# Optimization experiments

Hardware: AMD Instinct MI355X
Metric: run time of the kernel (lower is better)

The kernel has to match this reference:

```python
import jax, jax.numpy as jnp
import numpy as np
import math

B, T, C = 2, 2048, 1024
H = 16            # n_head
RATIO = 4         # ratio_kv
HKV = H // RATIO  # n_head_kv = 4
HD = C // H       # head_dim = 64
G = H // HKV      # query heads per kv head = 4


def _alibi_slopes(n_heads):
    # n_heads must be a power of 2 here (H=16)
    assert math.log2(n_heads).is_integer()
    start = 2.0 ** (-(2.0 ** (-(math.log2(n_heads) - 3))))
    return np.array([start * (start ** i) for i in range(n_heads)], dtype=np.float32)


def setup_inputs() -> dict:
    key = jax.random.key(0)
    ks = jax.random.split(key, 5)
    return {
        "x": jax.random.normal(ks[0], (B, T, C), dtype=jnp.float32),
        "Wq": jax.random.normal(ks[1], (C, C), dtype=jnp.float32) * 0.02,
        "Wk": jax.random.normal(ks[2], (C, HKV * HD), dtype=jnp.float32) * 0.02,
        "Wv": jax.random.normal(ks[3], (C, HKV * HD), dtype=jnp.float32) * 0.02,
        "Wo": jax.random.normal(ks[4], (C, C), dtype=jnp.float32) * 0.02,
    }


def reference(x, Wq, Wk, Wv, Wo):
    # GQA causal attention with ALiBi bias (flash-disabled fallback path).
    # q: [B,HKV,G,T,HD] (grouped query heads), k/v: [B,HKV,T,HD]
    q = (x @ Wq).reshape(B, T, H, HD).transpose(0, 2, 1, 3).reshape(B, HKV, G, T, HD)
    k = (x @ Wk).reshape(B, T, HKV, HD).transpose(0, 2, 1, 3)
    v = (x @ Wv).reshape(B, T, HKV, HD).transpose(0, 2, 1, 3)

    scale = 1.0 / math.sqrt(HD)
    att = jnp.einsum('bkgtd,bksd->bkgts', q, k) * scale  # [B,HKV,G,T,T]

    # ALiBi: original repeats alibi(n_head) by G and truncates to n_head,
    # so query head h uses slope get_slopes(H)[h // G] == slopes[:HKV] per kv group.
    slopes = jnp.asarray(_alibi_slopes(H))[:HKV]          # [HKV]
    pos = jnp.arange(T)
    rel = (pos[None, :] - pos[:, None]).astype(jnp.float32)  # [T,T], rel[i,j]=j-i
    bias = slopes[:, None, None] * rel                    # [HKV,T,T]
    causal = jnp.triu(jnp.full((T, T), -jnp.inf, dtype=jnp.float32), 1)

    att = att + bias[None, :, None] + causal
    att = jax.nn.softmax(att.astype(jnp.float32), axis=-1).astype(q.dtype)

    y = jnp.einsum('bkgts,bksd->bkgtd', att, v)           # [B,HKV,G,T,HD]
    y = y.reshape(B, H, T, HD).transpose(0, 2, 1, 3).reshape(B, T, C)
    return y @ Wo
```

## Files before the change

kernel.cpp:

```cpp
#include <hip/hip_runtime.h>
#include <hip/hip_bf16.h>
#include <math.h>

#define B_ 2
#define T_ 2048
#define C_ 1024
#define H_ 16
#define HKV_ 4
#define G_ 4
#define HD_ 64
#define KVC_ 256
#define NQKV_ 1536
#define NQT_ 32

typedef __attribute__((ext_vector_type(8))) short bf16x8;
typedef __attribute__((ext_vector_type(4))) float f32x4;

static __device__ inline short f2bf(float f) {
    __hip_bfloat16 h = __float2bfloat16(f);
    short s;
    __builtin_memcpy(&s, &h, 2);
    return s;
}
static __device__ inline short f2bf_trunc(float f) {
    unsigned int u;
    __builtin_memcpy(&u, &f, 4);
    return (short)(u >> 16);
}
static __device__ inline float bf2f(short s) {
    unsigned int u = ((unsigned int)(unsigned short)s) << 16;
    float f;
    __builtin_memcpy(&f, &u, 4);
    return f;
}

static __device__ inline void gload_lds16(const short* g, short* lds) {
    __builtin_amdgcn_global_load_lds(
        (const __attribute__((address_space(1))) unsigned int*)g,
        (__attribute__((address_space(3))) unsigned int*)lds, 16, 0, 0);
}

__global__ __launch_bounds__(256) void cast_bf16(
    const float* __restrict__ in, short* __restrict__ out, int n)
{
    const int i = (blockIdx.x * 256 + threadIdx.x) * 8;
    if (i >= n) return;
    const float4 a = *(const float4*)(in + i);
    const float4 b = *(const float4*)(in + i + 4);
    bf16x8 o;
    o[0] = f2bf(a.x); o[1] = f2bf(a.y); o[2] = f2bf(a.z); o[3] = f2bf(a.w);
    o[4] = f2bf(b.x); o[5] = f2bf(b.y); o[6] = f2bf(b.z); o[7] = f2bf(b.w);
    *(bf16x8*)(out + i) = o;
}

__global__ __launch_bounds__(256) void w_transpose(
    const float* __restrict__ Wq, const float* __restrict__ Wk,
    const float* __restrict__ Wv, const float* __restrict__ Wo,
    short* __restrict__ Wt, short* __restrict__ Wot)
{
    const int z = blockIdx.z;
    const float* in;
    short* out;
    int N;
    if (z == 0)      { in = Wq; out = Wt;                     N = C_; }
    else if (z == 1) { in = Wk; out = Wt + C_ * C_;           N = KVC_; }
    else if (z == 2) { in = Wv; out = Wt + (C_ + KVC_) * C_;  N = KVC_; }
    else             { in = Wo; out = Wot;                    N = C_; }
    const int n0 = blockIdx.x * 32;
    if (n0 >= N) return;
    __shared__ float t[32][33];
    const int tx = threadIdx.x, ty = threadIdx.y;
    const int k0 = blockIdx.y * 32;
    #pragma unroll
    for (int j = 0; j < 4; j++)
        t[ty + j * 8][tx] = in[(size_t)(k0 + ty + j * 8) * N + n0 + tx];
    __syncthreads();
    #pragma unroll
    for (int j = 0; j < 4; j++)
        out[(size_t)(n0 + ty + j * 8) * C_ + k0 + tx] = f2bf(t[tx][ty + j * 8]);
}

template <bool OUT_BF16>
__global__ __launch_bounds__(256) void gemm_bf16(
    const short* __restrict__ A, const short* __restrict__ Bt,
    void* __restrict__ Cout, int M, int N, int K)
{
    __shared__ short As[2][128 * 32];
    __shared__ short Bs[2][128 * 32];
    const int tid = threadIdx.x;
    const int wave = tid >> 6, lane = tid & 63;
    const int l15 = lane & 15, quad = lane >> 4;
    const int row0 = blockIdx.y * 128, col0 = blockIdx.x * 128;
    const int wr = (wave >> 1) * 64, wc = (wave & 1) * 64;
    const int sr = lane >> 2, kof = (lane & 3) * 8;

    f32x4 acc[4][4];
    #pragma unroll
    for (int i = 0; i < 4; i++)
        #pragma unroll
        for (int j = 0; j < 4; j++)
            acc[i][j] = (f32x4){0.f, 0.f, 0.f, 0.f};

#define GSTAGE(KT, BUF) do {                                                   \
        _Pragma("unroll")                                                      \
        for (int i_ = 0; i_ < 2; i_++) {                                       \
            const int rr = i_ * 64 + wave * 16;                                \
            gload_lds16(A + (size_t)(row0 + rr + sr) * K + (KT) + kof,         \
                        &As[BUF][rr * 32]);                                    \
            gload_lds16(Bt + (size_t)(col0 + rr + sr) * K + (KT) + kof,        \
                        &Bs[BUF][rr * 32]);                                    \
        }                                                                      \
    } while (0)

    GSTAGE(0, 0);
    asm volatile("s_waitcnt vmcnt(0)" ::: "memory");
    __builtin_amdgcn_s_barrier();

    int cur = 0;
    const int nkt = K >> 5;
    for (int t = 0; t < nkt; ++t) {
        if (t + 1 < nkt) GSTAGE((t + 1) * 32, cur ^ 1);

        bf16x8 af[4], bfr[4];
        #pragma unroll
        for (int mt = 0; mt < 4; mt++)
            af[mt] = *(const bf16x8*)&As[cur][(wr + mt * 16 + l15) * 32 + quad * 8];
        #pragma unroll
        for (int nt = 0; nt < 4; nt++)
            bfr[nt] = *(const bf16x8*)&Bs[cur][(wc + nt * 16 + l15) * 32 + quad * 8];
        #pragma unroll
        for (int mt = 0; mt < 4; mt++)
            #pragma unroll
            for (int nt = 0; nt < 4; nt++)
                acc[mt][nt] = __builtin_amdgcn_mfma_f32_16x16x32_bf16(
                    af[mt], bfr[nt], acc[mt][nt], 0, 0, 0);

        asm volatile("s_waitcnt vmcnt(0)" ::: "memory");
        __builtin_amdgcn_s_barrier();
        cur ^= 1;
    }
#undef GSTAGE

    #pragma unroll
    for (int mt = 0; mt < 4; mt++) {
        #pragma unroll
        for (int r = 0; r < 4; r++) {
            const size_t row = row0 + wr + mt * 16 + quad * 4 + r;
            #pragma unroll
            for (int nt = 0; nt < 4; nt++) {
                const size_t col = col0 + wc + nt * 16 + l15;
                if (OUT_BF16)
                    ((short*)Cout)[row * N + col] = f2bf(acc[mt][nt][r]);
                else
                    ((float*)Cout)[row * N + col] = acc[mt][nt][r];
            }
        }
    }
}

__global__ __launch_bounds__(256) void kv_tile(
    const short* __restrict__ QKV, short* __restrict__ Kt, short* __restrict__ Vt)
{
    __shared__ short Ls[64 * 72];
    const int jt = blockIdx.x;
    const int bk = blockIdx.y;
    const int b = bk >> 2, kh = bk & 3;
    const int tid = threadIdx.x;
    const int key = tid >> 2, d16 = (tid & 3) * 16;
    const size_t src = (size_t)(b * T_ + jt * 64 + key) * NQKV_ + C_ + kh * 64 + d16;
    const size_t tbase = (size_t)(bk * 32 + jt) * 4096;

    {
        const int i = (key >> 4) * 2 + (d16 >> 5);
        const int qd = (d16 & 31) >> 3;
        short* dst = Kt + tbase + i * 512 + (qd * 16 + (key & 15)) * 8;
        *(bf16x8*)dst         = *(const bf16x8*)(QKV + src);
        *(bf16x8*)(dst + 128) = *(const bf16x8*)(QKV + src + 8);
    }
    *(bf16x8*)&Ls[key * 72 + d16]     = *(const bf16x8*)(QKV + src + KVC_);
    *(bf16x8*)&Ls[key * 72 + d16 + 8] = *(const bf16x8*)(QKV + src + KVC_ + 8);
    __syncthreads();
    const int d = tid >> 2, k16 = (tid & 3) * 16;
    bf16x8 o0, o1;
    #pragma unroll
    for (int i = 0; i < 8; i++) o0[i] = Ls[(k16 + i) * 72 + d];
    #pragma unroll
    for (int i = 0; i < 8; i++) o1[i] = Ls[(k16 + 8 + i) * 72 + d];
    {
        const int i = (d >> 4) * 2 + (k16 >> 5);
        const int qk = (k16 & 31) >> 3;
        short* dst = Vt + tbase + i * 512 + (qk * 16 + (d & 15)) * 8;
        *(bf16x8*)dst         = o0;
        *(bf16x8*)(dst + 128) = o1;
    }
}

#define LSTR 72

__global__ __launch_bounds__(256) void attn_mfma(
    const short* __restrict__ QKV, const short* __restrict__ Ktg,
    const short* __restrict__ Vtg, short* __restrict__ Y)
{
    const int qx = blockIdx.x;
    const int bh = blockIdx.y;
    const int qtL = qx, qtH = NQT_ - 1 - qx;
    const int b = bh >> 4, h = bh & 15, kh = h >> 2;
    const float slope2 = exp2f(-0.5f * (float)(kh + 1)) * 1.44269504f;
    const int tid = threadIdx.x;
    const int wave = tid >> 6, lane = tid & 63;
    const int l15 = lane & 15, quad = lane >> 4;

    __shared__ short Ps[4 * 32 * LSTR];
    short* Pw = &Ps[wave * 32 * LSTR];
    const int wswz = ((quad >> 1) & 1) << 4;
    const int rswz = ((l15 >> 3) & 1) << 4;

    const size_t bT = (size_t)b * T_;
    const size_t tb0 = (size_t)((b * HKV_ + kh) * 32) * 4096;
    const short* Kt = Ktg + tb0;
    const short* Vt = Vtg + tb0;
    const int qrow0H = qtH * 64 + wave * 16;
    const int qrow0L = qtL * 64 + wave * 16;

    const float qscale = 0.125f * 1.44269504f;
    bf16x8 qfH[2], qfL[2];
    #pragma unroll
    for (int k0 = 0; k0 < 2; k0++) {
        const short* qpH = QKV + (bT + qrow0H + l15) * NQKV_ + h * 64;
        const short* qpL = QKV + (bT + qrow0L + l15) * NQKV_ + h * 64;
        bf16x8 rH = *(const bf16x8*)(qpH + k0 * 32 + quad * 8);
        bf16x8 rL = *(const bf16x8*)(qpL + k0 * 32 + quad * 8);
        #pragma unroll
        for (int j = 0; j < 8; j++) {
            qfH[k0][j] = f2bf(bf2f(rH[j]) * qscale);
            qfL[k0][j] = f2bf(bf2f(rL[j]) * qscale);
        }
    }

    const short one_s = (short)0x3F80;
    const bf16x8 ones = {one_s, one_s, one_s, one_s, one_s, one_s, one_s, one_s};

    f32x4 OaccH[4], OaccL[4], laccH, laccL;
    #pragma unroll
    for (int nt = 0; nt < 4; nt++) {
        OaccH[nt] = (f32x4){0.f, 0.f, 0.f, 0.f};
        OaccL[nt] = (f32x4){0.f, 0.f, 0.f, 0.f};
    }
    laccH = (f32x4){0.f, 0.f, 0.f, 0.f};
    laccL = (f32x4){0.f, 0.f, 0.f, 0.f};

    bf16x8 kf[8], vf[8];
    #pragma unroll
    for (int i = 0; i < 8; i++)
        kf[i] = *(const bf16x8*)(Kt + i * 512 + lane * 8);
    #pragma unroll
    for (int i = 0; i < 8; i++)
        vf[i] = *(const bf16x8*)(Vt + i * 512 + lane * 8);

    for (int jtk = 0; jtk <= qtH; jtk++) {
        const bool doL = (jtk <= qtL);
        const int pjt = (jtk < qtH) ? jtk + 1 : qtH;

        f32x4 sH[4], sL[4];
        #pragma unroll
        for (int nt = 0; nt < 4; nt++) {
            f32x4 a = {0.f, 0.f, 0.f, 0.f};
            a = __builtin_amdgcn_mfma_f32_16x16x32_bf16(qfH[0], kf[nt*2+0], a, 0, 0, 0);
            a = __builtin_amdgcn_mfma_f32_16x16x32_bf16(qfH[1], kf[nt*2+1], a, 0, 0, 0);
            sH[nt] = a;
        }
        if (doL) {
            #pragma unroll
            for (int nt = 0; nt < 4; nt++) {
                f32x4 a = {0.f, 0.f, 0.f, 0.f};
                a = __builtin_amdgcn_mfma_f32_16x16x32_bf16(qfL[0], kf[nt*2+0], a, 0, 0, 0);
                a = __builtin_amdgcn_mfma_f32_16x16x32_bf16(qfL[1], kf[nt*2+1], a, 0, 0, 0);
                sL[nt] = a;
            }
        }

        #pragma unroll
        for (int i = 0; i < 8; i++)
            kf[i] = *(const bf16x8*)(Kt + (size_t)pjt * 4096 + i * 512 + lane * 8);

        {
            const float base = slope2 * (float)(jtk * 64 + l15 - quad * 4 - qrow0H);
            if (jtk == qtH) {
                #pragma unroll
                for (int nt = 0; nt < 4; nt++) {
                    const int colsw = ((nt * 16 + l15) ^ wswz);
                    #pragma unroll
                    for (int r = 0; r < 4; r++) {
                        const float relv = (float)(jtk * 64 + l15 - quad * 4 - qrow0H)
                                         + (float)(nt * 16 - r);
                        float p = __builtin_amdgcn_exp2f(
                            fmaf(slope2, (float)(nt * 16 - r), base) + sH[nt][r]);
                        if (relv > 0.f) p = 0.f;
                        Pw[(quad * 4 + r) * LSTR + colsw] = f2bf_trunc(p);
                    }
                }
            } else {
                #pragma unroll
                for (int nt = 0; nt < 4; nt++) {
                    const int colsw = ((nt * 16 + l15) ^ wswz);
                    #pragma unroll
                    for (int r = 0; r < 4; r++) {
                        float p = __builtin_amdgcn_exp2f(
                            fmaf(slope2, (float)(nt * 16 - r), base) + sH[nt][r]);
                        Pw[(quad * 4 + r) * LSTR + colsw] = f2bf_trunc(p);
                    }
                }
            }
        }
        if (doL) {
            const float base = slope2 * (float)(jtk * 64 + l15 - quad * 4 - qrow0L);
            if (jtk == qtL) {
                #pragma unroll
                for (int nt = 0; nt < 4; nt++) {
                    const int colsw = ((nt * 16 + l15) ^ wswz);
                    #pragma unroll
                    for (int r = 0; r < 4; r++) {
                        const float relv = (float)(jtk * 64 + l15 - quad * 4 - qrow0L)
                                         + (float)(nt * 16 - r);
                        float p = __builtin_amdgcn_exp2f(
                            fmaf(slope2, (float)(nt * 16 - r), base) + sL[nt][r]);
                        if (relv > 0.f) p = 0.f;
                        Pw[(16 + quad * 4 + r) * LSTR + colsw] = f2bf_trunc(p);
                    }
                }
            } else {
                #pragma unroll
                for (int nt = 0; nt < 4; nt++) {
                    const int colsw = ((nt * 16 + l15) ^ wswz);
                    #pragma unroll
                    for (int r = 0; r < 4; r++) {
                        float p = __builtin_amdgcn_exp2f(
                            fmaf(slope2, (float)(nt * 16 - r), base) + sL[nt][r]);
                        Pw[(16 + quad * 4 + r) * LSTR + colsw] = f2bf_trunc(p);
                    }
                }
            }
        }
        __asm__ volatile("s_waitcnt lgkmcnt(0)" ::: "memory");

        {
            bf16x8 pf0 = *(const bf16x8*)&Pw[l15 * LSTR + ((quad * 8) ^ rswz)];
            bf16x8 pf1 = *(const bf16x8*)&Pw[l15 * LSTR + ((32 + quad * 8) ^ rswz)];
            laccH = __builtin_amdgcn_mfma_f32_16x16x32_bf16(pf0, ones, laccH, 0, 0, 0);
            laccH = __builtin_amdgcn_mfma_f32_16x16x32_bf16(pf1, ones, laccH, 0, 0, 0);
            #pragma unroll
            for (int nt = 0; nt < 4; nt++) {
                OaccH[nt] = __builtin_amdgcn_mfma_f32_16x16x32_bf16(
                    pf0, vf[nt*2+0], OaccH[nt], 0, 0, 0);
                OaccH[nt] = __builtin_amdgcn_mfma_f32_16x16x32_bf16(
                    pf1, vf[nt*2+1], OaccH[nt], 0, 0, 0);
            }
        }
        if (doL) {
            bf16x8 pf0 = *(const bf16x8*)&Pw[(16 + l15) * LSTR + ((quad * 8) ^ rswz)];
            bf16x8 pf1 = *(const bf16x8*)&Pw[(16 + l15) * LSTR + ((32 + quad * 8) ^ rswz)];
            laccL = __builtin_amdgcn_mfma_f32_16x16x32_bf16(pf0, ones, laccL, 0, 0, 0);
            laccL = __builtin_amdgcn_mfma_f32_16x16x32_bf16(pf1, ones, laccL, 0, 0, 0);
            #pragma unroll
            for (int nt = 0; nt < 4; nt++) {
                OaccL[nt] = __builtin_amdgcn_mfma_f32_16x16x32_bf16(
                    pf0, vf[nt*2+0], OaccL[nt], 0, 0, 0);
                OaccL[nt] = __builtin_amdgcn_mfma_f32_16x16x32_bf16(
                    pf1, vf[nt*2+1], OaccL[nt], 0, 0, 0);
            }
        }

        #pragma unroll
        for (int i = 0; i < 8; i++)
            vf[i] = *(const bf16x8*)(Vt + (size_t)pjt * 4096 + i * 512 + lane * 8);
    }

    #pragma unroll
    for (int r = 0; r < 4; r++) {
        const float invH = 1.f / laccH[r];
        const float invL = 1.f / laccL[r];
        const int rowH = qrow0H + quad * 4 + r;
        const int rowL = qrow0L + quad * 4 + r;
        short* ypH = Y + (bT + rowH) * C_ + h * 64 + l15;
        short* ypL = Y + (bT + rowL) * C_ + h * 64 + l15;
        #pragma unroll
        for (int nt = 0; nt < 4; nt++) {
            ypH[nt * 16] = f2bf(OaccH[nt][r] * invH);
            ypL[nt * 16] = f2bf(OaccL[nt][r] * invL);
        }
    }
}

extern "C" void kernel_launch(void* const* d_in, const int* in_sizes, int n_in,
                              void* d_out, int out_size, void* d_ws, size_t ws_size,
                              hipStream_t stream) {
    const float* x  = (const float*)d_in[0];
    const float* Wq = (const float*)d_in[1];
    const float* Wk = (const float*)d_in[2];
    const float* Wv = (const float*)d_in[3];
    const float* Wo = (const float*)d_in[4];
    float* out = (float*)d_out;

    const int M = B_ * T_;
    short* xb  = (short*)d_ws;
    short* Wt  = xb  + (size_t)M * C_;
    short* Wot = Wt  + (size_t)NQKV_ * C_;
    short* QKV = Wot + (size_t)C_ * C_;
    short* Yb  = QKV + (size_t)M * NQKV_;
    short* Ktg = Yb  + (size_t)M * C_;
    short* Vtg = Ktg + (size_t)8 * 32 * 4096;

    cast_bf16<<<dim3(M * C_ / (256 * 8)), dim3(256), 0, stream>>>(x, xb, M * C_);
    w_transpose<<<dim3(32, 32, 4), dim3(32, 8), 0, stream>>>(Wq, Wk, Wv, Wo, Wt, Wot);

    gemm_bf16<true><<<dim3(NQKV_ / 128, M / 128), dim3(256), 0, stream>>>(
        xb, Wt, QKV, M, NQKV_, C_);
    kv_tile<<<dim3(32, 8), dim3(256), 0, stream>>>(QKV, Ktg, Vtg);
    attn_mfma<<<dim3(NQT_ / 2, B_ * H_), dim3(256), 0, stream>>>(QKV, Ktg, Vtg, Yb);
    gemm_bf16<false><<<dim3(C_ / 128, M / 128), dim3(256), 0, stream>>>(
        Yb, Wot, out, M, C_, C_);
}
```

Measured before the change: 172.2 us.

## Process one query tile per attention block instead of paired high/low tiles

The attention kernel no longer pairs a high and a low causal query tile in one block for load balance. Each block now handles a single 64-row query tile, launching twice as many blocks with the heaviest tiles scheduled first. It also asks for 4 blocks per CU via launch bounds and halves the P staging buffer in shared memory. The intent is higher occupancy and fewer registers per thread. The cost is that K/V tiles shared by the pair are now loaded twice, and per-block work is uneven under the causal mask.

Result: slower. 198.7 us (+15.4%).

```diff
diff --git a/kernel.cpp b/kernel.cpp
--- a/kernel.cpp
+++ b/kernel.cpp
@@ -197,21 +197,20 @@
 
 #define LSTR 72
 
-__global__ __launch_bounds__(256) void attn_mfma(
+__global__ __launch_bounds__(256, 4) void attn_mfma(
     const short* __restrict__ QKV, const short* __restrict__ Ktg,
     const short* __restrict__ Vtg, short* __restrict__ Y)
 {
-    const int qx = blockIdx.x;
+    const int qt = NQT_ - 1 - blockIdx.x;
     const int bh = blockIdx.y;
-    const int qtL = qx, qtH = NQT_ - 1 - qx;
     const int b = bh >> 4, h = bh & 15, kh = h >> 2;
     const float slope2 = exp2f(-0.5f * (float)(kh + 1)) * 1.44269504f;
     const int tid = threadIdx.x;
     const int wave = tid >> 6, lane = tid & 63;
     const int l15 = lane & 15, quad = lane >> 4;
 
-    __shared__ short Ps[4 * 32 * LSTR];
-    short* Pw = &Ps[wave * 32 * LSTR];
+    __shared__ short Ps[4 * 16 * LSTR];
+    short* Pw = &Ps[wave * 16 * LSTR];
     const int wswz = ((quad >> 1) & 1) << 4;
     const int rswz = ((l15 >> 3) & 1) << 4;
 
@@ -219,35 +218,27 @@
     const size_t tb0 = (size_t)((b * HKV_ + kh) * 32) * 4096;
     const short* Kt = Ktg + tb0;
     const short* Vt = Vtg + tb0;
-    const int qrow0H = qtH * 64 + wave * 16;
-    const int qrow0L = qtL * 64 + wave * 16;
+    const int qrow0 = qt * 64 + wave * 16;
 
     const float qscale = 0.125f * 1.44269504f;
-    bf16x8 qfH[2], qfL[2];
+    bf16x8 qf[2];
     #pragma unroll
     for (int k0 = 0; k0 < 2; k0++) {
-        const short* qpH = QKV + (bT + qrow0H + l15) * NQKV_ + h * 64;
-        const short* qpL = QKV + (bT + qrow0L + l15) * NQKV_ + h * 64;
-        bf16x8 rH = *(const bf16x8*)(qpH + k0 * 32 + quad * 8);
-        bf16x8 rL = *(const bf16x8*)(qpL + k0 * 32 + quad * 8);
-        #pragma unroll
-        for (int j = 0; j < 8; j++) {
-            qfH[k0][j] = f2bf(bf2f(rH[j]) * qscale);
-            qfL[k0][j] = f2bf(bf2f(rL[j]) * qscale);
-        }
+        const short* qp = QKV + (bT + qrow0 + l15) * NQKV_ + h * 64;
+        bf16x8 r = *(const bf16x8*)(qp + k0 * 32 + quad * 8);
+        #pragma unroll
+        for (int j = 0; j < 8; j++)
+            qf[k0][j] = f2bf(bf2f(r[j]) * qscale);
     }
 
     const short one_s = (short)0x3F80;
     const bf16x8 ones = {one_s, one_s, one_s, one_s, one_s, one_s, one_s, one_s};
 
-    f32x4 OaccH[4], OaccL[4], laccH, laccL;
-    #pragma unroll
-    for (int nt = 0; nt < 4; nt++) {
-        OaccH[nt] = (f32x4){0.f, 0.f, 0.f, 0.f};
-        OaccL[nt] = (f32x4){0.f, 0.f, 0.f, 0.f};
-    }
-    laccH = (f32x4){0.f, 0.f, 0.f, 0.f};
-    laccL = (f32x4){0.f, 0.f, 0.f, 0.f};
+    f32x4 Oacc[4], lacc;
+    #pragma unroll
+    for (int nt = 0; nt < 4; nt++)
+        Oacc[nt] = (f32x4){0.f, 0.f, 0.f, 0.f};
+    lacc = (f32x4){0.f, 0.f, 0.f, 0.f};
 
     bf16x8 kf[8], vf[8];
     #pragma unroll
@@ -257,26 +248,16 @@
     for (int i = 0; i < 8; i++)
         vf[i] = *(const bf16x8*)(Vt + i * 512 + lane * 8);
 
-    for (int jtk = 0; jtk <= qtH; jtk++) {
-        const bool doL = (jtk <= qtL);
-        const int pjt = (jtk < qtH) ? jtk + 1 : qtH;
-
-        f32x4 sH[4], sL[4];
+    for (int jtk = 0; jtk <= qt; jtk++) {
+        const int pjt = (jtk < qt) ? jtk + 1 : qt;
+
+        f32x4 s[4];
         #pragma unroll
         for (int nt = 0; nt < 4; nt++) {
             f32x4 a = {0.f, 0.f, 0.f, 0.f};
-            a = __builtin_amdgcn_mfma_f32_16x16x32_bf16(qfH[0], kf[nt*2+0], a, 0, 0, 0);
-            a = __builtin_amdgcn_mfma_f32_16x16x32_bf16(qfH[1], kf[nt*2+1], a, 0, 0, 0);
-            sH[nt] = a;
-        }
-        if (doL) {
-            #pragma unroll
-            for (int nt = 0; nt < 4; nt++) {
-                f32x4 a = {0.f, 0.f, 0.f, 0.f};
-                a = __builtin_amdgcn_mfma_f32_16x16x32_bf16(qfL[0], kf[nt*2+0], a, 0, 0, 0);
-                a = __builtin_amdgcn_mfma_f32_16x16x32_bf16(qfL[1], kf[nt*2+1], a, 0, 0, 0);
-                sL[nt] = a;
-            }
+            a = __builtin_amdgcn_mfma_f32_16x16x32_bf16(qf[0], kf[nt*2+0], a, 0, 0, 0);
+            a = __builtin_amdgcn_mfma_f32_16x16x32_bf16(qf[1], kf[nt*2+1], a, 0, 0, 0);
+            s[nt] = a;
         }
 
         #pragma unroll
@@ -284,17 +265,17 @@
             kf[i] = *(const bf16x8*)(Kt + (size_t)pjt * 4096 + i * 512 + lane * 8);
 
         {
-            const float base = slope2 * (float)(jtk * 64 + l15 - quad * 4 - qrow0H);
-            if (jtk == qtH) {
+            const float base = slope2 * (float)(jtk * 64 + l15 - quad * 4 - qrow0);
+            if (jtk == qt) {
                 #pragma unroll
                 for (int nt = 0; nt < 4; nt++) {
                     const int colsw = ((nt * 16 + l15) ^ wswz);
                     #pragma unroll
                     for (int r = 0; r < 4; r++) {
-                        const float relv = (float)(jtk * 64 + l15 - quad * 4 - qrow0H)
+                        const float relv = (float)(jtk * 64 + l15 - quad * 4 - qrow0)
                                          + (float)(nt * 16 - r);
                         float p = __builtin_amdgcn_exp2f(
-                            fmaf(slope2, (float)(nt * 16 - r), base) + sH[nt][r]);
+                            fmaf(slope2, (float)(nt * 16 - r), base) + s[nt][r]);
                         if (relv > 0.f) p = 0.f;
                         Pw[(quad * 4 + r) * LSTR + colsw] = f2bf_trunc(p);
                     }
@@ -306,69 +287,27 @@
                     #pragma unroll
                     for (int r = 0; r < 4; r++) {
                         float p = __builtin_amdgcn_exp2f(
-                            fmaf(slope2, (float)(nt * 16 - r), base) + sH[nt][r]);
+                            fmaf(slope2, (float)(nt * 16 - r), base) + s[nt][r]);
                         Pw[(quad * 4 + r) * LSTR + colsw] = f2bf_trunc(p);
                     }
                 }
             }
         }
-        if (doL) {
-            const float base = slope2 * (float)(jtk * 64 + l15 - quad * 4 - qrow0L);
-            if (jtk == qtL) {
-                #pragma unroll
-                for (int nt = 0; nt < 4; nt++) {
-                    const int colsw = ((nt * 16 + l15) ^ wswz);
-                    #pragma unroll
-                    for (int r = 0; r < 4; r++) {
-                        const float relv = (float)(jtk * 64 + l15 - quad * 4 - qrow0L)
-                                         + (float)(nt * 16 - r);
-                        float p = __builtin_amdgcn_exp2f(
-                            fmaf(slope2, (float)(nt * 16 - r), base) + sL[nt][r]);
-                        if (relv > 0.f) p = 0.f;
-                        Pw[(16 + quad * 4 + r) * LSTR + colsw] = f2bf_trunc(p);
-                    }
-                }
-            } else {
-                #pragma unroll
-                for (int nt = 0; nt < 4; nt++) {
-                    const int colsw = ((nt * 16 + l15) ^ wswz);
-                    #pragma unroll
-                    for (int r = 0; r < 4; r++) {
-                        float p = __builtin_amdgcn_exp2f(
-                            fmaf(slope2, (float)(nt * 16 - r), base) + sL[nt][r]);
-                        Pw[(16 + quad * 4 + r) * LSTR + colsw] = f2bf_trunc(p);
-                    }
-                }
-            }
-        }
         __asm__ volatile("s_waitcnt lgkmcnt(0)" ::: "memory");
 
         {
             bf16x8 pf0 = *(const bf16x8*)&Pw[l15 * LSTR + ((quad * 8) ^ rswz)];
             bf16x8 pf1 = *(const bf16x8*)&Pw[l15 * LSTR + ((32 + quad * 8) ^ rswz)];
-            laccH = __builtin_amdgcn_mfma_f32_16x16x32_bf16(pf0, ones, laccH, 0, 0, 0);
-            laccH = __builtin_amdgcn_mfma_f32_16x16x32_bf16(pf1, ones, laccH, 0, 0, 0);
+            lacc = __builtin_amdgcn_mfma_f32_16x16x32_bf16(pf0, ones, lacc, 0, 0, 0);
+            lacc = __builtin_amdgcn_mfma_f32_16x16x32_bf16(pf1, ones, lacc, 0, 0, 0);
             #pragma unroll
             for (int nt = 0; nt < 4; nt++) {
-                OaccH[nt] = __builtin_amdgcn_mfma_f32_16x16x32_bf16(
-                    pf0, vf[nt*2+0], OaccH[nt], 0, 0, 0);
-                OaccH[nt] = __builtin_amdgcn_mfma_f32_16x16x32_bf16(
-                    pf1, vf[nt*2+1], OaccH[nt], 0, 0, 0);
+                Oacc[nt] = __builtin_amdgcn_mfma_f32_16x16x32_bf16(
+                    pf0, vf[nt*2+0], Oacc[nt], 0, 0, 0);
+                Oacc[nt] = __builtin_amdgcn_mfma_f32_16x16x32_bf16(
+                    pf1, vf[nt*2+1], Oacc[nt], 0, 0, 0);
             }
         }
-        if (doL) {
-            bf16x8 pf0 = *(const bf16x8*)&Pw[(16 + l15) * LSTR + ((quad * 8) ^ rswz)];
-            bf16x8 pf1 = *(const bf16x8*)&Pw[(16 + l15) * LSTR + ((32 + quad * 8) ^ rswz)];
-            laccL = __builtin_amdgcn_mfma_f32_16x16x32_bf16(pf0, ones, laccL, 0, 0, 0);
-            laccL = __builtin_amdgcn_mfma_f32_16x16x32_bf16(pf1, ones, laccL, 0, 0, 0);
-            #pragma unroll
-            for (int nt = 0; nt < 4; nt++) {
-                OaccL[nt] = __builtin_amdgcn_mfma_f32_16x16x32_bf16(
-                    pf0, vf[nt*2+0], OaccL[nt], 0, 0, 0);
-                OaccL[nt] = __builtin_amdgcn_mfma_f32_16x16x32_bf16(
-                    pf1, vf[nt*2+1], OaccL[nt], 0, 0, 0);
-            }
-        }
 
         #pragma unroll
         for (int i = 0; i < 8; i++)
@@ -377,17 +316,12 @@
 
     #pragma unroll
     for (int r = 0; r < 4; r++) {
-        const float invH = 1.f / laccH[r];
-        const float invL = 1.f / laccL[r];
-        const int rowH = qrow0H + quad * 4 + r;
-        const int rowL = qrow0L + quad * 4 + r;
-        short* ypH = Y + (bT + rowH) * C_ + h * 64 + l15;
-        short* ypL = Y + (bT + rowL) * C_ + h * 64 + l15;
-        #pragma unroll
-        for (int nt = 0; nt < 4; nt++) {
-            ypH[nt * 16] = f2bf(OaccH[nt][r] * invH);
-            ypL[nt * 16] = f2bf(OaccL[nt][r] * invL);
-        }
+        const float inv = 1.f / lacc[r];
+        const int row = qrow0 + quad * 4 + r;
+        short* yp = Y + (bT + row) * C_ + h * 64 + l15;
+        #pragma unroll
+        for (int nt = 0; nt < 4; nt++)
+            yp[nt * 16] = f2bf(Oacc[nt][r] * inv);
     }
 }
 
@@ -416,7 +350,7 @@
     gemm_bf16<true><<<dim3(NQKV_ / 128, M / 128), dim3(256), 0, stream>>>(
         xb, Wt, QKV, M, NQKV_, C_);
     kv_tile<<<dim3(32, 8), dim3(256), 0, stream>>>(QKV, Ktg, Vtg);
-    attn_mfma<<<dim3(NQT_ / 2, B_ * H_), dim3(256), 0, stream>>>(QKV, Ktg, Vtg, Yb);
+    attn_mfma<<<dim3(NQT_, B_ * H_), dim3(256), 0, stream>>>(QKV, Ktg, Vtg, Yb);
     gemm_bf16<false><<<dim3(C_ / 128, M / 128), dim3(256), 0, stream>>>(
         Yb, Wot, out, M, C_, C_);
 }
```
